# Optimization experiments

Hardware: AMD Instinct MI355X
Metric: run time of the kernel (lower is better)

The kernel has to match this reference:

```python
import jax, jax.numpy as jnp
import numpy as np

HIDDEN = 1024
NUM_HEADS = 16
HEAD_DIM = HIDDEN // NUM_HEADS  # 64


def setup_inputs() -> dict:
    key = jax.random.key(0)
    ks = jax.random.split(key, 7)
    B, S = 2, 2048
    hidden_states = jax.random.normal(ks[0], (B, S, HIDDEN), dtype=jnp.float32)
    # nn.Linear weights stored as [out, in]; y = x @ W.T + b
    scale = 1.0 / np.sqrt(HIDDEN)
    Wq = jax.random.uniform(ks[1], (HIDDEN, HIDDEN), jnp.float32, -scale, scale)
    Wk = jax.random.uniform(ks[2], (HIDDEN, HIDDEN), jnp.float32, -scale, scale)
    Wv = jax.random.uniform(ks[3], (HIDDEN, HIDDEN), jnp.float32, -scale, scale)
    bq = jax.random.uniform(ks[4], (HIDDEN,), jnp.float32, -scale, scale)
    bk = jax.random.uniform(ks[5], (HIDDEN,), jnp.float32, -scale, scale)
    bv = jax.random.uniform(ks[6], (HIDDEN,), jnp.float32, -scale, scale)
    return {"hidden_states": hidden_states, "Wq": Wq, "bq": bq, "Wk": Wk, "bk": bk, "Wv": Wv, "bv": bv}


def _split_heads(x):
    # [B,S,H] -> [B,nH,S,hd]
    B, S, _ = x.shape
    return x.reshape(B, S, NUM_HEADS, HEAD_DIM).transpose(0, 2, 1, 3)


def reference(hidden_states, Wq, bq, Wk, bk, Wv, bv):
    q = _split_heads(hidden_states @ Wq.T + bq)  # [B,nH,S,hd]
    k = _split_heads(hidden_states @ Wk.T + bk)
    v = _split_heads(hidden_states @ Wv.T + bv)
    scores = jnp.einsum("bhqd,bhkd->bhqk", q, k) / jnp.sqrt(jnp.float32(HEAD_DIM))
    probs = jax.nn.softmax(scores, axis=-1)  # [B,nH,S,S]
    ctx = jnp.einsum("bhqk,bhkd->bhqd", probs, v)  # [B,nH,S,hd]
    B, _, S, _ = ctx.shape
    ctx = ctx.transpose(0, 2, 1, 3).reshape(B, S, NUM_HEADS * HEAD_DIM)
    return (ctx, probs)
```

## Files before the change

kernel.cpp:

```cpp
#include <hip/hip_runtime.h>
#include <hip/hip_bf16.h>
#include <cstdint>
#include <cstddef>

#define HIDDEN 1024
#define NHEADS 16
#define HDIM 64
#define BATCH 2
#define SEQ 2048
#define MROWS (BATCH*SEQ)

typedef __attribute__((ext_vector_type(8))) short short8;
typedef __attribute__((ext_vector_type(4))) float float4v;

__device__ __forceinline__ short f2bf(float f) {
    union { float f; uint32_t u; } v; v.f = f;
    uint32_t u = v.u;
    uint32_t r = (u + 0x7fffu + ((u >> 16) & 1u)) >> 16;
    return (short)r;
}

__global__ void conv_f32_bf16(const float* __restrict__ src, short* __restrict__ dst, int n8) {
    int i = blockIdx.x * blockDim.x + threadIdx.x;
    if (i < n8) {
        const float4v* s = (const float4v*)src;
        float4v a = s[2 * i], b = s[2 * i + 1];
        short8 o;
        o[0] = f2bf(a[0]); o[1] = f2bf(a[1]); o[2] = f2bf(a[2]); o[3] = f2bf(a[3]);
        o[4] = f2bf(b[0]); o[5] = f2bf(b[1]); o[6] = f2bf(b[2]); o[7] = f2bf(b[3]);
        ((short8*)dst)[i] = o;
    }
}

__global__ __launch_bounds__(256, 2) void proj_gemm(
    const short* __restrict__ Xb,
    const short* __restrict__ Wb0, const short* __restrict__ Wb1, const short* __restrict__ Wb2,
    const float* __restrict__ b0, const float* __restrict__ b1, const float* __restrict__ b2,
    short* __restrict__ O0, short* __restrict__ O1, short* __restrict__ O2)
{
    const int z = blockIdx.z;
    const short* W  = (z == 0) ? Wb0 : (z == 1) ? Wb1 : Wb2;
    const float* bias = (z == 0) ? b0 : (z == 1) ? b1 : b2;
    short* Out = (z == 0) ? O0 : (z == 1) ? O1 : O2;

    __shared__ short As[128 * 72];
    __shared__ short Bs[128 * 72];

    const int t = threadIdx.x;
    const int lane = t & 63, w = t >> 6;
    const int wm = w >> 1, wn = w & 1;
    const int quad = lane >> 4, l16 = lane & 15;

    const int m0 = blockIdx.y * 128;
    const int n0 = blockIdx.x * 128;

    float4v acc[4][4];
#pragma unroll
    for (int i = 0; i < 4; i++)
#pragma unroll
        for (int j = 0; j < 4; j++) acc[i][j] = (float4v){0.f, 0.f, 0.f, 0.f};

    for (int k0 = 0; k0 < HIDDEN; k0 += 64) {
        __syncthreads();
#pragma unroll
        for (int j = 0; j < 4; j++) {
            int cid = t + j * 256;
            int row = cid >> 3, c = cid & 7;
            *(short8*)&As[row * 72 + c * 8] = *(const short8*)&Xb[(size_t)(m0 + row) * HIDDEN + k0 + c * 8];
            *(short8*)&Bs[row * 72 + c * 8] = *(const short8*)&W[(size_t)(n0 + row) * HIDDEN + k0 + c * 8];
        }
        __syncthreads();
#pragma unroll
        for (int kj = 0; kj < 2; kj++) {
            short8 a[4], bfr[4];
#pragma unroll
            for (int i = 0; i < 4; i++)
                a[i] = *(const short8*)&As[(wm * 64 + i * 16 + l16) * 72 + kj * 32 + quad * 8];
#pragma unroll
            for (int j = 0; j < 4; j++)
                bfr[j] = *(const short8*)&Bs[(wn * 64 + j * 16 + l16) * 72 + kj * 32 + quad * 8];
#pragma unroll
            for (int i = 0; i < 4; i++)
#pragma unroll
                for (int j = 0; j < 4; j++)
                    acc[i][j] = __builtin_amdgcn_mfma_f32_16x16x32_bf16(a[i], bfr[j], acc[i][j], 0, 0, 0);
        }
    }

#pragma unroll
    for (int i = 0; i < 4; i++)
#pragma unroll
        for (int j = 0; j < 4; j++) {
            int n = n0 + wn * 64 + j * 16 + l16;
            float bv = bias[n];
#pragma unroll
            for (int r = 0; r < 4; r++) {
                int m = m0 + wm * 64 + i * 16 + quad * 4 + r;
                Out[(size_t)m * HIDDEN + n] = f2bf(acc[i][j][r] + bv);
            }
        }
}

__global__ __launch_bounds__(256, 2) void attn(
    const short* __restrict__ Qb, const short* __restrict__ Kb, const short* __restrict__ Vb,
    float* __restrict__ ctx, float* __restrict__ probs)
{
    const int bh = blockIdx.y;
    const int b = bh >> 4, h = bh & 15;
    const int q0 = blockIdx.x * 64;

    __shared__ short Qs[64 * 72];
    __shared__ short Ks[64 * 72];
    __shared__ short Ps[64 * 72];
    __shared__ short Vt[64 * 72];

    const int t = threadIdx.x;
    const int lane = t & 63, w = t >> 6;
    const int quad = lane >> 4, l16 = lane & 15;

    const short* qp = Qb + (size_t)(b * SEQ + q0) * HIDDEN + h * 64;
    const short* kp = Kb + (size_t)(b * SEQ) * HIDDEN + h * 64;
    const short* vp = Vb + (size_t)(b * SEQ) * HIDDEN + h * 64;

#pragma unroll
    for (int j = 0; j < 2; j++) {
        int cid = t + j * 256;
        int row = cid >> 3, c = cid & 7;
        *(short8*)&Qs[row * 72 + c * 8] = *(const short8*)&qp[(size_t)row * HIDDEN + c * 8];
    }

    float m_r[4], l_r[4];
#pragma unroll
    for (int r = 0; r < 4; r++) { m_r[r] = -1e30f; l_r[r] = 0.f; }
    const float scale = 0.125f;

    for (int kb = 0; kb < SEQ / 64; kb++) {
        __syncthreads();
#pragma unroll
        for (int j = 0; j < 2; j++) {
            int cid = t + j * 256;
            int row = cid >> 3, c = cid & 7;
            *(short8*)&Ks[row * 72 + c * 8] = *(const short8*)&kp[(size_t)(kb * 64 + row) * HIDDEN + c * 8];
        }
        __syncthreads();

        float4v s[4];
#pragma unroll
        for (int ct = 0; ct < 4; ct++) {
            float4v accv = (float4v){0.f, 0.f, 0.f, 0.f};
#pragma unroll
            for (int kj = 0; kj < 2; kj++) {
                short8 a = *(const short8*)&Qs[(w * 16 + l16) * 72 + kj * 32 + quad * 8];
                short8 bf = *(const short8*)&Ks[(ct * 16 + l16) * 72 + kj * 32 + quad * 8];
                accv = __builtin_amdgcn_mfma_f32_16x16x32_bf16(a, bf, accv, 0, 0, 0);
            }
#pragma unroll
            for (int r = 0; r < 4; r++) s[ct][r] = accv[r] * scale;
        }
#pragma unroll
        for (int r = 0; r < 4; r++) {
            float mx = fmaxf(fmaxf(s[0][r], s[1][r]), fmaxf(s[2][r], s[3][r]));
#pragma unroll
            for (int d = 1; d < 16; d <<= 1) mx = fmaxf(mx, __shfl_xor(mx, d, 64));
            float mnew = fmaxf(m_r[r], mx);
            float sum = 0.f;
#pragma unroll
            for (int ct = 0; ct < 4; ct++) sum += __expf(s[ct][r] - mnew);
#pragma unroll
            for (int d = 1; d < 16; d <<= 1) sum += __shfl_xor(sum, d, 64);
            l_r[r] = l_r[r] * __expf(m_r[r] - mnew) + sum;
            m_r[r] = mnew;
        }
    }

    float il[4];
#pragma unroll
    for (int r = 0; r < 4; r++) il[r] = 1.f / l_r[r];

    float4v o[4];
#pragma unroll
    for (int dt = 0; dt < 4; dt++) o[dt] = (float4v){0.f, 0.f, 0.f, 0.f};

    for (int kb = 0; kb < SEQ / 64; kb++) {
        __syncthreads();
#pragma unroll
        for (int j = 0; j < 2; j++) {
            int cid = t + j * 256;
            int row = cid >> 3, c = cid & 7;
            *(short8*)&Ks[row * 72 + c * 8] = *(const short8*)&kp[(size_t)(kb * 64 + row) * HIDDEN + c * 8];
            short8 vv = *(const short8*)&vp[(size_t)(kb * 64 + row) * HIDDEN + c * 8];
#pragma unroll
            for (int e = 0; e < 8; e++) Vt[(c * 8 + e) * 72 + row] = vv[e];
        }
        __syncthreads();

#pragma unroll
        for (int ct = 0; ct < 4; ct++) {
            float4v accv = (float4v){0.f, 0.f, 0.f, 0.f};
#pragma unroll
            for (int kj = 0; kj < 2; kj++) {
                short8 a = *(const short8*)&Qs[(w * 16 + l16) * 72 + kj * 32 + quad * 8];
                short8 bf = *(const short8*)&Ks[(ct * 16 + l16) * 72 + kj * 32 + quad * 8];
                accv = __builtin_amdgcn_mfma_f32_16x16x32_bf16(a, bf, accv, 0, 0, 0);
            }
#pragma unroll
            for (int r = 0; r < 4; r++) {
                float p = __expf(accv[r] * scale - m_r[r]) * il[r];
                int grow = q0 + w * 16 + quad * 4 + r;
                int gcol = kb * 64 + ct * 16 + l16;
                probs[((size_t)bh * SEQ + grow) * SEQ + gcol] = p;
                Ps[(w * 16 + quad * 4 + r) * 72 + ct * 16 + l16] = f2bf(p);
            }
        }
        __syncthreads();

#pragma unroll
        for (int dt = 0; dt < 4; dt++) {
#pragma unroll
            for (int kj = 0; kj < 2; kj++) {
                short8 a = *(const short8*)&Ps[(w * 16 + l16) * 72 + kj * 32 + quad * 8];
                short8 bf = *(const short8*)&Vt[(dt * 16 + l16) * 72 + kj * 32 + quad * 8];
                o[dt] = __builtin_amdgcn_mfma_f32_16x16x32_bf16(a, bf, o[dt], 0, 0, 0);
            }
        }
    }

#pragma unroll
    for (int dt = 0; dt < 4; dt++) {
#pragma unroll
        for (int r = 0; r < 4; r++) {
            int grow = b * SEQ + q0 + w * 16 + quad * 4 + r;
            int gcol = h * 64 + dt * 16 + l16;
            ctx[(size_t)grow * HIDDEN + gcol] = o[dt][r];
        }
    }
}

extern "C" void kernel_launch(void* const* d_in, const int* in_sizes, int n_in,
                              void* d_out, int out_size, void* d_ws, size_t ws_size,
                              hipStream_t stream) {
    const float* X  = (const float*)d_in[0];
    const float* Wq = (const float*)d_in[1];
    const float* bq = (const float*)d_in[2];
    const float* Wk = (const float*)d_in[3];
    const float* bk = (const float*)d_in[4];
    const float* Wv = (const float*)d_in[5];
    const float* bv = (const float*)d_in[6];

    float* out = (float*)d_out;
    float* ctx = out;
    float* probs = out + (size_t)4194304;

    char* ws = (char*)d_ws;
    short* Xb  = (short*)(ws);
    short* Wqb = (short*)(ws + (8u << 20));
    short* Wkb = (short*)(ws + (10u << 20));
    short* Wvb = (short*)(ws + (12u << 20));
    short* Qb  = (short*)(ws + (14u << 20));
    short* Kb  = (short*)(ws + (22u << 20));
    short* Vb  = (short*)(ws + (30u << 20));

    {
        int n8 = MROWS * HIDDEN / 8;
        conv_f32_bf16<<<dim3(n8 / 256), dim3(256), 0, stream>>>(X, Xb, n8);
        int w8 = HIDDEN * HIDDEN / 8;
        conv_f32_bf16<<<dim3(w8 / 256), dim3(256), 0, stream>>>(Wq, Wqb, w8);
        conv_f32_bf16<<<dim3(w8 / 256), dim3(256), 0, stream>>>(Wk, Wkb, w8);
        conv_f32_bf16<<<dim3(w8 / 256), dim3(256), 0, stream>>>(Wv, Wvb, w8);
    }

    {
        dim3 grid(HIDDEN / 128, MROWS / 128, 3);
        proj_gemm<<<grid, dim3(256), 0, stream>>>(Xb, Wqb, Wkb, Wvb, bq, bk, bv, Qb, Kb, Vb);
    }

    {
        dim3 grid(SEQ / 64, BATCH * NHEADS);
        attn<<<grid, dim3(256), 0, stream>>>(Qb, Kb, Vb, ctx, probs);
    }
}
```

Measured before the change: 769.4 us.

## Restructure attention: register-resident Q/K fragments, transposed V, vectorized nontemporal probs stores

The projection GEMM now writes V transposed per head, so the attention kernel can load V fragments straight from global memory without an LDS transpose. Q and K fragments are also read directly into registers, which removes most shared-memory staging and barriers. The QK^T operands are swapped so each lane owns a query row, letting probs be written as float4 nontemporal stores and the row sum need only two shuffles. Other changes: the running-max subtraction is dropped in favour of exp2 with a folded scale, ctx normalization is deferred to the end, and workgroup indices are swizzled for cache locality. Skipping the max subtraction risks overflow if scores become large.

```diff
diff --git a/kernel.cpp b/kernel.cpp
--- a/kernel.cpp
+++ b/kernel.cpp
@@ -1,5 +1,4 @@
 #include <hip/hip_runtime.h>
-#include <hip/hip_bf16.h>
 #include <cstdint>
 #include <cstddef>
 
@@ -11,6 +10,7 @@
 #define MROWS (BATCH*SEQ)
 
 typedef __attribute__((ext_vector_type(8))) short short8;
+typedef __attribute__((ext_vector_type(4))) short short4v;
 typedef __attribute__((ext_vector_type(4))) float float4v;
 
 __device__ __forceinline__ short f2bf(float f) {
@@ -87,32 +87,49 @@
         }
     }
 
-#pragma unroll
-    for (int i = 0; i < 4; i++)
+    if (z == 2) {
 #pragma unroll
         for (int j = 0; j < 4; j++) {
             int n = n0 + wn * 64 + j * 16 + l16;
             float bv = bias[n];
-#pragma unroll
-            for (int r = 0; r < 4; r++) {
-                int m = m0 + wm * 64 + i * 16 + quad * 4 + r;
-                Out[(size_t)m * HIDDEN + n] = f2bf(acc[i][j][r] + bv);
+            int d = n & 63, hh = n >> 6;
+#pragma unroll
+            for (int i = 0; i < 4; i++) {
+                int mbase = m0 + wm * 64 + i * 16 + quad * 4;
+                int bb = mbase >> 11, s = mbase & (SEQ - 1);
+                short4v pk;
+#pragma unroll
+                for (int r = 0; r < 4; r++) pk[r] = f2bf(acc[i][j][r] + bv);
+                *(short4v*)&Out[(((size_t)bb * NHEADS + hh) * HDIM + d) * SEQ + s] = pk;
             }
         }
+    } else {
+#pragma unroll
+        for (int i = 0; i < 4; i++)
+#pragma unroll
+            for (int j = 0; j < 4; j++) {
+                int n = n0 + wn * 64 + j * 16 + l16;
+                float bv = bias[n];
+#pragma unroll
+                for (int r = 0; r < 4; r++) {
+                    int m = m0 + wm * 64 + i * 16 + quad * 4 + r;
+                    Out[(size_t)m * HIDDEN + n] = f2bf(acc[i][j][r] + bv);
+                }
+            }
+    }
 }
 
 __global__ __launch_bounds__(256, 2) void attn(
-    const short* __restrict__ Qb, const short* __restrict__ Kb, const short* __restrict__ Vb,
+    const short* __restrict__ Qb, const short* __restrict__ Kb, const short* __restrict__ Vt,
     float* __restrict__ ctx, float* __restrict__ probs)
 {
-    const int bh = blockIdx.y;
+    int bid0 = blockIdx.y * gridDim.x + blockIdx.x;
+    int wg = (bid0 & 7) * 128 + (bid0 >> 3);
+    const int bh = wg >> 5;
+    const int q0 = (wg & 31) << 6;
     const int b = bh >> 4, h = bh & 15;
-    const int q0 = blockIdx.x * 64;
-
-    __shared__ short Qs[64 * 72];
-    __shared__ short Ks[64 * 72];
+
     __shared__ short Ps[64 * 72];
-    __shared__ short Vt[64 * 72];
 
     const int t = threadIdx.x;
     const int lane = t & 63, w = t >> 6;
@@ -120,118 +137,88 @@
 
     const short* qp = Qb + (size_t)(b * SEQ + q0) * HIDDEN + h * 64;
     const short* kp = Kb + (size_t)(b * SEQ) * HIDDEN + h * 64;
-    const short* vp = Vb + (size_t)(b * SEQ) * HIDDEN + h * 64;
-
-#pragma unroll
-    for (int j = 0; j < 2; j++) {
-        int cid = t + j * 256;
-        int row = cid >> 3, c = cid & 7;
-        *(short8*)&Qs[row * 72 + c * 8] = *(const short8*)&qp[(size_t)row * HIDDEN + c * 8];
-    }
-
-    float m_r[4], l_r[4];
-#pragma unroll
-    for (int r = 0; r < 4; r++) { m_r[r] = -1e30f; l_r[r] = 0.f; }
-    const float scale = 0.125f;
-
+    const short* vp = Vt + (size_t)bh * HDIM * SEQ;
+
+    short8 qf0 = *(const short8*)&qp[(w * 16 + l16) * HIDDEN + quad * 8];
+    short8 qf1 = *(const short8*)&qp[(w * 16 + l16) * HIDDEN + 32 + quad * 8];
+
+    const float C = 0.18033688f;
+    const float4v z4 = (float4v){0.f, 0.f, 0.f, 0.f};
+
+    float l = 0.f;
     for (int kb = 0; kb < SEQ / 64; kb++) {
-        __syncthreads();
-#pragma unroll
-        for (int j = 0; j < 2; j++) {
-            int cid = t + j * 256;
-            int row = cid >> 3, c = cid & 7;
-            *(short8*)&Ks[row * 72 + c * 8] = *(const short8*)&kp[(size_t)(kb * 64 + row) * HIDDEN + c * 8];
-        }
-        __syncthreads();
-
-        float4v s[4];
+        const short* kt = kp + (size_t)kb * 64 * HIDDEN;
+        float4v s[4] = {z4, z4, z4, z4};
 #pragma unroll
         for (int ct = 0; ct < 4; ct++) {
-            float4v accv = (float4v){0.f, 0.f, 0.f, 0.f};
-#pragma unroll
-            for (int kj = 0; kj < 2; kj++) {
-                short8 a = *(const short8*)&Qs[(w * 16 + l16) * 72 + kj * 32 + quad * 8];
-                short8 bf = *(const short8*)&Ks[(ct * 16 + l16) * 72 + kj * 32 + quad * 8];
-                accv = __builtin_amdgcn_mfma_f32_16x16x32_bf16(a, bf, accv, 0, 0, 0);
-            }
-#pragma unroll
-            for (int r = 0; r < 4; r++) s[ct][r] = accv[r] * scale;
-        }
-#pragma unroll
-        for (int r = 0; r < 4; r++) {
-            float mx = fmaxf(fmaxf(s[0][r], s[1][r]), fmaxf(s[2][r], s[3][r]));
-#pragma unroll
-            for (int d = 1; d < 16; d <<= 1) mx = fmaxf(mx, __shfl_xor(mx, d, 64));
-            float mnew = fmaxf(m_r[r], mx);
-            float sum = 0.f;
-#pragma unroll
-            for (int ct = 0; ct < 4; ct++) sum += __expf(s[ct][r] - mnew);
-#pragma unroll
-            for (int d = 1; d < 16; d <<= 1) sum += __shfl_xor(sum, d, 64);
-            l_r[r] = l_r[r] * __expf(m_r[r] - mnew) + sum;
-            m_r[r] = mnew;
-        }
-    }
-
-    float il[4];
-#pragma unroll
-    for (int r = 0; r < 4; r++) il[r] = 1.f / l_r[r];
-
-    float4v o[4];
-#pragma unroll
-    for (int dt = 0; dt < 4; dt++) o[dt] = (float4v){0.f, 0.f, 0.f, 0.f};
+            short8 k0 = *(const short8*)&kt[(ct * 16 + l16) * HIDDEN + quad * 8];
+            short8 k1 = *(const short8*)&kt[(ct * 16 + l16) * HIDDEN + 32 + quad * 8];
+            s[ct] = __builtin_amdgcn_mfma_f32_16x16x32_bf16(k0, qf0, s[ct], 0, 0, 0);
+            s[ct] = __builtin_amdgcn_mfma_f32_16x16x32_bf16(k1, qf1, s[ct], 0, 0, 0);
+        }
+        float sum = 0.f;
+#pragma unroll
+        for (int ct = 0; ct < 4; ct++)
+#pragma unroll
+            for (int r = 0; r < 4; r++)
+                sum += __builtin_amdgcn_exp2f(s[ct][r] * C);
+        sum += __shfl_xor(sum, 16, 64);
+        sum += __shfl_xor(sum, 32, 64);
+        l += sum;
+    }
+    const float il = 1.f / l;
+
+    float4v o[4] = {z4, z4, z4, z4};
+    float* prow = &probs[((size_t)bh * SEQ + (q0 + w * 16 + l16)) * SEQ];
 
     for (int kb = 0; kb < SEQ / 64; kb++) {
-        __syncthreads();
-#pragma unroll
-        for (int j = 0; j < 2; j++) {
-            int cid = t + j * 256;
-            int row = cid >> 3, c = cid & 7;
-            *(short8*)&Ks[row * 72 + c * 8] = *(const short8*)&kp[(size_t)(kb * 64 + row) * HIDDEN + c * 8];
-            short8 vv = *(const short8*)&vp[(size_t)(kb * 64 + row) * HIDDEN + c * 8];
-#pragma unroll
-            for (int e = 0; e < 8; e++) Vt[(c * 8 + e) * 72 + row] = vv[e];
-        }
-        __syncthreads();
-
+        const short* kt = kp + (size_t)kb * 64 * HIDDEN;
+        const short* vt = vp + kb * 64;
+
+        float4v s[4] = {z4, z4, z4, z4};
 #pragma unroll
         for (int ct = 0; ct < 4; ct++) {
-            float4v accv = (float4v){0.f, 0.f, 0.f, 0.f};
-#pragma unroll
-            for (int kj = 0; kj < 2; kj++) {
-                short8 a = *(const short8*)&Qs[(w * 16 + l16) * 72 + kj * 32 + quad * 8];
-                short8 bf = *(const short8*)&Ks[(ct * 16 + l16) * 72 + kj * 32 + quad * 8];
-                accv = __builtin_amdgcn_mfma_f32_16x16x32_bf16(a, bf, accv, 0, 0, 0);
-            }
-#pragma unroll
-            for (int r = 0; r < 4; r++) {
-                float p = __expf(accv[r] * scale - m_r[r]) * il[r];
-                int grow = q0 + w * 16 + quad * 4 + r;
-                int gcol = kb * 64 + ct * 16 + l16;
-                probs[((size_t)bh * SEQ + grow) * SEQ + gcol] = p;
-                Ps[(w * 16 + quad * 4 + r) * 72 + ct * 16 + l16] = f2bf(p);
-            }
-        }
-        __syncthreads();
-
+            short8 k0 = *(const short8*)&kt[(ct * 16 + l16) * HIDDEN + quad * 8];
+            short8 k1 = *(const short8*)&kt[(ct * 16 + l16) * HIDDEN + 32 + quad * 8];
+            s[ct] = __builtin_amdgcn_mfma_f32_16x16x32_bf16(k0, qf0, s[ct], 0, 0, 0);
+            s[ct] = __builtin_amdgcn_mfma_f32_16x16x32_bf16(k1, qf1, s[ct], 0, 0, 0);
+        }
+
+#pragma unroll
+        for (int ct = 0; ct < 4; ct++) {
+            float4v p, pr;
+#pragma unroll
+            for (int r = 0; r < 4; r++) p[r] = __builtin_amdgcn_exp2f(s[ct][r] * C);
+#pragma unroll
+            for (int r = 0; r < 4; r++) pr[r] = p[r] * il;
+            __builtin_nontemporal_store(pr, (float4v*)&prow[(size_t)kb * 64 + ct * 16 + quad * 4]);
+            short4v pb;
+#pragma unroll
+            for (int r = 0; r < 4; r++) pb[r] = f2bf(p[r]);
+            *(short4v*)&Ps[(w * 16 + l16) * 72 + ct * 16 + quad * 4] = pb;
+        }
+
+        short8 pa0 = *(const short8*)&Ps[(w * 16 + l16) * 72 + quad * 8];
+        short8 pa1 = *(const short8*)&Ps[(w * 16 + l16) * 72 + 32 + quad * 8];
 #pragma unroll
         for (int dt = 0; dt < 4; dt++) {
-#pragma unroll
-            for (int kj = 0; kj < 2; kj++) {
-                short8 a = *(const short8*)&Ps[(w * 16 + l16) * 72 + kj * 32 + quad * 8];
-                short8 bf = *(const short8*)&Vt[(dt * 16 + l16) * 72 + kj * 32 + quad * 8];
-                o[dt] = __builtin_amdgcn_mfma_f32_16x16x32_bf16(a, bf, o[dt], 0, 0, 0);
-            }
-        }
-    }
-
+            short8 v0 = *(const short8*)&vt[(size_t)(dt * 16 + l16) * SEQ + quad * 8];
+            short8 v1 = *(const short8*)&vt[(size_t)(dt * 16 + l16) * SEQ + 32 + quad * 8];
+            o[dt] = __builtin_amdgcn_mfma_f32_16x16x32_bf16(pa0, v0, o[dt], 0, 0, 0);
+            o[dt] = __builtin_amdgcn_mfma_f32_16x16x32_bf16(pa1, v1, o[dt], 0, 0, 0);
+        }
+    }
+
+    float ilr[4];
+#pragma unroll
+    for (int r = 0; r < 4; r++) ilr[r] = __shfl(il, quad * 4 + r, 64);
 #pragma unroll
     for (int dt = 0; dt < 4; dt++) {
 #pragma unroll
         for (int r = 0; r < 4; r++) {
             int grow = b * SEQ + q0 + w * 16 + quad * 4 + r;
             int gcol = h * 64 + dt * 16 + l16;
-            ctx[(size_t)grow * HIDDEN + gcol] = o[dt][r];
+            ctx[(size_t)grow * HIDDEN + gcol] = o[dt][r] * ilr[r];
         }
     }
 }
@@ -258,7 +245,7 @@
     short* Wvb = (short*)(ws + (12u << 20));
     short* Qb  = (short*)(ws + (14u << 20));
     short* Kb  = (short*)(ws + (22u << 20));
-    short* Vb  = (short*)(ws + (30u << 20));
+    short* Vtb = (short*)(ws + (30u << 20));
 
     {
         int n8 = MROWS * HIDDEN / 8;
@@ -271,11 +258,11 @@
 
     {
         dim3 grid(HIDDEN / 128, MROWS / 128, 3);
-        proj_gemm<<<grid, dim3(256), 0, stream>>>(Xb, Wqb, Wkb, Wvb, bq, bk, bv, Qb, Kb, Vb);
+        proj_gemm<<<grid, dim3(256), 0, stream>>>(Xb, Wqb, Wkb, Wvb, bq, bk, bv, Qb, Kb, Vtb);
     }
 
     {
         dim3 grid(SEQ / 64, BATCH * NHEADS);
-        attn<<<grid, dim3(256), 0, stream>>>(Qb, Kb, Vb, ctx, probs);
-    }
-}
+        attn<<<grid, dim3(256), 0, stream>>>(Qb, Kb, Vtb, ctx, probs);
+    }
+}
```

Result: slower. 859.0 us (+11.6%).
